# Optimization experiments

Measured on AMD Instinct MI355X. Metric: run time of the kernel, lower is better.

Reference implementation:

```python
import jax, jax.numpy as jnp
import numpy as np

B, T, D, H, E, L = 128, 200, 256, 4, 4, 2
HD = D // H
ITEM = 50000


def _ln(x, s, b):
    m = x.mean(-1, keepdims=True)
    v = ((x - m) ** 2).mean(-1, keepdims=True)
    return (x - m) / jnp.sqrt(v + 1e-8) * s + b


def setup_inputs() -> dict:
    key = jax.random.key(0)
    ks = jax.random.split(key, 20)
    n = lambda k, sh: jax.random.normal(k, sh, jnp.float32) * 0.02
    inp = {}
    inp['log_seqs'] = jax.random.randint(ks[0], (B, T), 0, ITEM + 1)
    inp['pos_seqs'] = jax.random.randint(ks[1], (B, T), 0, ITEM + 1)
    inp['neg_seqs'] = jax.random.randint(ks[2], (B, T), 0, ITEM + 1)
    inp['expert_ids'] = jax.random.randint(ks[3], (B,), 0, E)
    inp['item_emb'] = n(ks[4], (ITEM + 1, D)).at[0].set(0.0)  # padding_idx=0
    inp['pos_emb'] = n(ks[5], (T + 1, D)).at[0].set(0.0)
    inp['attn_ln_s'] = jnp.ones((L, D), jnp.float32)
    inp['attn_ln_b'] = jnp.zeros((L, D), jnp.float32)
    inp['in_w'] = n(ks[6], (L, E, 3 * D, D))
    inp['in_b'] = jnp.zeros((L, E, 3 * D), jnp.float32)
    inp['out_w'] = n(ks[7], (L, E, D, D))
    inp['out_b'] = jnp.zeros((L, E, D), jnp.float32)
    inp['fwd_ln_s'] = jnp.ones((L, D), jnp.float32)
    inp['fwd_ln_b'] = jnp.zeros((L, D), jnp.float32)
    inp['ffn_w1'] = n(ks[8], (L, D, D))
    inp['ffn_b1'] = jnp.zeros((L, D), jnp.float32)
    inp['ffn_w2'] = n(ks[9], (L, D, D))
    inp['ffn_b2'] = jnp.zeros((L, D), jnp.float32)
    inp['last_ln_s'] = jnp.ones((D,), jnp.float32)
    inp['last_ln_b'] = jnp.zeros((D,), jnp.float32)
    return inp


def reference(log_seqs, pos_seqs, neg_seqs, expert_ids, item_emb, pos_emb,
              attn_ln_s, attn_ln_b, in_w, in_b, out_w, out_b,
              fwd_ln_s, fwd_ln_b, ffn_w1, ffn_b1, ffn_w2, ffn_b2,
              last_ln_s, last_ln_b):
    seqs = item_emb[log_seqs] * jnp.float32(np.sqrt(D))          # [B,T,D]
    poss = jnp.arange(1, T + 1)[None, :] * (log_seqs != 0)       # pos ids, 0 where pad
    seqs = seqs + pos_emb[poss]
    causal = jnp.tril(jnp.ones((T, T), bool))
    scale = jnp.float32(1.0 / np.sqrt(HD))

    for l in range(L):
        qn = _ln(seqs, attn_ln_s[l], attn_ln_b[l])               # query is LN'd; K,V are not
        wq, wk, wv = in_w[l, :, :D], in_w[l, :, D:2 * D], in_w[l, :, 2 * D:]
        bq, bk, bv = in_b[l, :, :D], in_b[l, :, D:2 * D], in_b[l, :, 2 * D:]
        q = jnp.einsum('btd,efd->ebtf', qn, wq) + bq[:, None, None, :]
        k = jnp.einsum('btd,efd->ebtf', seqs, wk) + bk[:, None, None, :]
        v = jnp.einsum('btd,efd->ebtf', seqs, wv) + bv[:, None, None, :]
        q = q.reshape(E, B, T, H, HD)
        k = k.reshape(E, B, T, H, HD)
        v = v.reshape(E, B, T, H, HD)
        scores = jnp.einsum('ebqhd,ebkhd->ebhqk', q, k) * scale  # [E,B,H,T,T]
        scores = jnp.where(causal, scores, jnp.float32(-1e9))
        attn = jax.nn.softmax(scores, axis=-1)
        o = jnp.einsum('ebhqk,ebkhd->ebqhd', attn, v).reshape(E, B, T, D)
        o = jnp.einsum('ebtd,efd->ebtf', o, out_w[l]) + out_b[l][:, None, None, :]
        gated = o[expert_ids, jnp.arange(B)]                     # hard one-hot gate -> [B,T,D]
        seqs = qn + gated
        seqs = _ln(seqs, fwd_ln_s[l], fwd_ln_b[l])
        h = jax.nn.relu(seqs @ ffn_w1[l].T + ffn_b1[l])
        seqs = seqs + (h @ ffn_w2[l].T + ffn_b2[l])

    feats = _ln(seqs, last_ln_s, last_ln_b)                      # [B,T,D]
    pos_logits = (feats * item_emb[pos_seqs]).sum(-1)            # [B,T]
    neg_logits = (feats * item_emb[neg_seqs]).sum(-1)
    return (pos_logits, neg_logits)
```

## Files before the change

kernel.cpp:

```cpp
#include <hip/hip_runtime.h>
#include <hip/hip_bf16.h>

namespace {

typedef unsigned short ushort;
constexpr int B  = 128;
constexpr int T  = 200;
constexpr int D  = 256;
constexpr int H  = 4;
constexpr int NE = 4;
constexpr int NL = 2;
constexpr int HD = 64;
constexpr int BT = B * T;

constexpr int BM = 64;
constexpr int BK = 64;
constexpr int MT = (T + BM - 1) / BM;
constexpr int HS = 264;

typedef __bf16 bf16x8 __attribute__((ext_vector_type(8)));
typedef float f32x4 __attribute__((ext_vector_type(4)));
typedef unsigned short ushort8v __attribute__((ext_vector_type(8)));

__device__ inline float wave_sum(float x) {
#pragma unroll
  for (int off = 32; off > 0; off >>= 1) x += __shfl_xor(x, off);
  return x;
}
__device__ inline unsigned int f2bf(float x) {
  unsigned int u = __float_as_uint(x);
  return (u + 0x7fffu + ((u >> 16) & 1u)) >> 16;
}
__device__ inline ushort f2bfs(float x) { return (ushort)f2bf(x); }
__device__ inline float bf2f(ushort u) {
  return __uint_as_float((unsigned int)u << 16);
}
__device__ inline bf16x8 ldb8(const ushort* p) {
  return __builtin_bit_cast(bf16x8, *(const ushort8v*)p);
}

__global__ void k_cvt(const float* __restrict__ src, ushort* __restrict__ dst,
                      int n4) {
  int i = blockIdx.x * 256 + threadIdx.x;
  if (i < n4) {
    float4 v = ((const float4*)src)[i];
    ushort4 u;
    u.x = f2bfs(v.x); u.y = f2bfs(v.y); u.z = f2bfs(v.z); u.w = f2bfs(v.w);
    ((ushort4*)dst)[i] = u;
  }
}

__global__ __launch_bounds__(256) void k_embed_ln(
    const int* __restrict__ log_seqs, const float* __restrict__ item_emb,
    const float* __restrict__ pos_emb, const float* __restrict__ lns,
    const float* __restrict__ lnb, ushort* __restrict__ seqs,
    ushort* __restrict__ qn) {
  int tok = blockIdx.x * 4 + (threadIdx.x >> 6);
  int lane = threadIdx.x & 63;
  int t = tok % T;
  int idx = log_seqs[tok];
  int pos = (idx != 0) ? (t + 1) : 0;
  float4 iv = ((const float4*)(item_emb + (size_t)idx * D))[lane];
  float4 pv = ((const float4*)(pos_emb + (size_t)pos * D))[lane];
  float v0 = iv.x * 16.0f + pv.x;
  float v1 = iv.y * 16.0f + pv.y;
  float v2 = iv.z * 16.0f + pv.z;
  float v3 = iv.w * 16.0f + pv.w;
  ushort4 r;
  r.x = f2bfs(v0); r.y = f2bfs(v1); r.z = f2bfs(v2); r.w = f2bfs(v3);
  ((ushort4*)(seqs + (size_t)tok * D))[lane] = r;
  float mean = wave_sum(v0 + v1 + v2 + v3) * (1.0f / D);
  float c0 = v0 - mean, c1 = v1 - mean, c2 = v2 - mean, c3 = v3 - mean;
  float var = wave_sum(c0 * c0 + c1 * c1 + c2 * c2 + c3 * c3) * (1.0f / D);
  float inv = rsqrtf(var + 1e-8f);
  float4 sv = ((const float4*)lns)[lane];
  float4 bv = ((const float4*)lnb)[lane];
  ushort4 o;
  o.x = f2bfs(c0 * inv * sv.x + bv.x);
  o.y = f2bfs(c1 * inv * sv.y + bv.y);
  o.z = f2bfs(c2 * inv * sv.z + bv.z);
  o.w = f2bfs(c3 * inv * sv.w + bv.w);
  ((ushort4*)(qn + (size_t)tok * D))[lane] = o;
}

template <int ROWS>
__device__ inline void stage_bf16(const ushort* __restrict__ src, int ld,
                                  int valid, int k0, ushort* __restrict__ dst,
                                  int tid) {
#pragma unroll
  for (int p = 0; p < ROWS * 8 / 256; p++) {
    int slot = p * 256 + tid;
    int r = slot >> 3, s_st = slot & 7;
    int s_src = s_st ^ (r & 7);
    int rs = (r < valid) ? r : (valid - 1);
    uint4 w = *(const uint4*)(src + (size_t)rs * ld + k0 + s_src * 8);
    *(uint4*)(dst + r * BK + s_st * 8) = w;
  }
}
__device__ inline bf16x8 frag(const ushort* tile, int row, int slot_log) {
  int s = slot_log ^ (row & 7);
  return ldb8(tile + row * BK + s * 8);
}

__global__ __launch_bounds__(256) void k_gemm_qkv(
    const ushort* __restrict__ qn, const ushort* __restrict__ seqs,
    const ushort* __restrict__ w, const float* __restrict__ bias,
    const int* __restrict__ expert_ids,
    ushort* __restrict__ q, ushort* __restrict__ k, ushort* __restrict__ v) {
  constexpr int NWG = B * MT * 6;
  int phys = blockIdx.x;
  int bid = (phys & 7) * (NWG >> 3) + (phys >> 3);
  int nt = bid % 6;
  int mt = (bid / 6) % MT;
  int b  = bid / (6 * MT);
  int e = expert_ids[b];
  int m0 = mt * BM;
  int valid = min(BM, T - m0);
  const ushort* X = (nt < 2) ? qn : seqs;
  const ushort* Xb = X + (size_t)(b * T + m0) * D;
  const ushort* Wb = w + (size_t)e * 3 * D * D + (size_t)nt * 128 * D;

  __shared__ __align__(16) ushort Xl[BM * BK];
  __shared__ __align__(16) ushort Wl[128 * BK];
  int tid = threadIdx.x, wv = tid >> 6, lane = tid & 63;
  int g = lane >> 4, lm = lane & 15;

  f32x4 acc[4][2];
#pragma unroll
  for (int mi = 0; mi < 4; mi++)
#pragma unroll
    for (int ni = 0; ni < 2; ni++) acc[mi][ni] = (f32x4){0.f, 0.f, 0.f, 0.f};

  for (int kt = 0; kt < D / BK; kt++) {
    stage_bf16<BM>(Xb, D, valid, kt * BK, Xl, tid);
    stage_bf16<128>(Wb, D, 128, kt * BK, Wl, tid);
    __syncthreads();
    bf16x8 a[4][2], bb[2][2];
#pragma unroll
    for (int mi = 0; mi < 4; mi++)
#pragma unroll
      for (int hh = 0; hh < 2; hh++)
        a[mi][hh] = frag(Xl, mi * 16 + lm, hh * 4 + g);
#pragma unroll
    for (int ni = 0; ni < 2; ni++)
#pragma unroll
      for (int hh = 0; hh < 2; hh++)
        bb[ni][hh] = frag(Wl, wv * 32 + ni * 16 + lm, hh * 4 + g);
#pragma unroll
    for (int mi = 0; mi < 4; mi++)
#pragma unroll
      for (int ni = 0; ni < 2; ni++) {
        acc[mi][ni] = __builtin_amdgcn_mfma_f32_16x16x32_bf16(a[mi][0], bb[ni][0],
                                                              acc[mi][ni], 0, 0, 0);
        acc[mi][ni] = __builtin_amdgcn_mfma_f32_16x16x32_bf16(a[mi][1], bb[ni][1],
                                                              acc[mi][ni], 0, 0, 0);
      }
    __syncthreads();
  }

  ushort* outb = (nt < 2) ? q : (nt < 4 ? k : v);
  size_t rowbase = (size_t)(b * T + m0);
#pragma unroll
  for (int mi = 0; mi < 4; mi++) {
#pragma unroll
    for (int ni = 0; ni < 2; ni++) {
      int col = (nt & 1) * 128 + wv * 32 + ni * 16 + lm;
      float bbv = bias[e * 3 * D + nt * 128 + wv * 32 + ni * 16 + lm];
#pragma unroll
      for (int r = 0; r < 4; r++) {
        int lr = mi * 16 + 4 * g + r;
        if (lr < valid)
          outb[(rowbase + lr) * D + col] = f2bfs(acc[mi][ni][r] + bbv);
      }
    }
  }
}

__global__ __launch_bounds__(256) void k_oproj(
    const ushort* __restrict__ o, const ushort* __restrict__ qn,
    const ushort* __restrict__ w, const float* __restrict__ bo,
    const float* __restrict__ lns, const float* __restrict__ lnb,
    const int* __restrict__ expert_ids, ushort* __restrict__ seqs) {
  int bid = blockIdx.x;
  int mt = bid % MT;
  int b  = bid / MT;
  int e = expert_ids[b];
  int m0 = mt * BM;
  int valid = min(BM, T - m0);
  const ushort* Xb = o + (size_t)(b * T + m0) * D;
  const ushort* Wb = w + (size_t)e * D * D;

  __shared__ __align__(16) ushort Xl[BM * BK];
  __shared__ __align__(16) ushort Wl[D * BK];
  __shared__ float rs_sum[BM][4];
  __shared__ float rs_sq[BM][4];
  int tid = threadIdx.x, wv = tid >> 6, lane = tid & 63;
  int g = lane >> 4, lm = lane & 15;

  f32x4 acc[4][4];
#pragma unroll
  for (int mi = 0; mi < 4; mi++)
#pragma unroll
    for (int ni = 0; ni < 4; ni++) acc[mi][ni] = (f32x4){0.f, 0.f, 0.f, 0.f};

  for (int kt = 0; kt < D / BK; kt++) {
    stage_bf16<BM>(Xb, D, valid, kt * BK, Xl, tid);
    stage_bf16<D>(Wb, D, D, kt * BK, Wl, tid);
    __syncthreads();
    bf16x8 a[4][2], bb[4][2];
#pragma unroll
    for (int mi = 0; mi < 4; mi++)
#pragma unroll
      for (int hh = 0; hh < 2; hh++)
        a[mi][hh] = frag(Xl, mi * 16 + lm, hh * 4 + g);
#pragma unroll
    for (int ni = 0; ni < 4; ni++)
#pragma unroll
      for (int hh = 0; hh < 2; hh++)
        bb[ni][hh] = frag(Wl, wv * 64 + ni * 16 + lm, hh * 4 + g);
#pragma unroll
    for (int mi = 0; mi < 4; mi++)
#pragma unroll
      for (int ni = 0; ni < 4; ni++) {
        acc[mi][ni] = __builtin_amdgcn_mfma_f32_16x16x32_bf16(a[mi][0], bb[ni][0],
                                                              acc[mi][ni], 0, 0, 0);
        acc[mi][ni] = __builtin_amdgcn_mfma_f32_16x16x32_bf16(a[mi][1], bb[ni][1],
                                                              acc[mi][ni], 0, 0, 0);
      }
    __syncthreads();
  }

  size_t rowbase = (size_t)(b * T + m0);
#pragma unroll
  for (int ni = 0; ni < 4; ni++) {
    int col = wv * 64 + ni * 16 + lm;
    float bbv = bo[e * D + col];
#pragma unroll
    for (int mi = 0; mi < 4; mi++)
#pragma unroll
      for (int r = 0; r < 4; r++) {
        int lr = mi * 16 + 4 * g + r;
        int lrc = (lr < valid) ? lr : (valid - 1);
        acc[mi][ni][r] += bbv + bf2f(qn[(rowbase + lrc) * D + col]);
      }
  }
#pragma unroll
  for (int mi = 0; mi < 4; mi++)
#pragma unroll
    for (int r = 0; r < 4; r++) {
      float s = 0.f, q2 = 0.f;
#pragma unroll
      for (int ni = 0; ni < 4; ni++) {
        float x = acc[mi][ni][r];
        s += x; q2 += x * x;
      }
#pragma unroll
      for (int off = 1; off < 16; off <<= 1) {
        s += __shfl_xor(s, off);
        q2 += __shfl_xor(q2, off);
      }
      if (lm == 0) {
        int row = mi * 16 + 4 * g + r;
        rs_sum[row][wv] = s;
        rs_sq[row][wv] = q2;
      }
    }
  __syncthreads();
  float scv[4], bcv[4];
#pragma unroll
  for (int ni = 0; ni < 4; ni++) {
    int col = wv * 64 + ni * 16 + lm;
    scv[ni] = lns[col];
    bcv[ni] = lnb[col];
  }
#pragma unroll
  for (int mi = 0; mi < 4; mi++)
#pragma unroll
    for (int r = 0; r < 4; r++) {
      int lr = mi * 16 + 4 * g + r;
      float4 s4 = *(const float4*)rs_sum[lr];
      float4 q4 = *(const float4*)rs_sq[lr];
      float mean = (s4.x + s4.y + s4.z + s4.w) * (1.0f / D);
      float var = (q4.x + q4.y + q4.z + q4.w) * (1.0f / D) - mean * mean;
      float rstd = rsqrtf(fmaxf(var, 0.f) + 1e-8f);
      if (lr < valid) {
#pragma unroll
        for (int ni = 0; ni < 4; ni++) {
          int col = wv * 64 + ni * 16 + lm;
          float lnv = (acc[mi][ni][r] - mean) * rstd * scv[ni] + bcv[ni];
          seqs[(rowbase + lr) * D + col] = f2bfs(lnv);
        }
      }
    }
}

__global__ __launch_bounds__(256) void k_ffn(
    const ushort* __restrict__ xin, const ushort* __restrict__ w1,
    const float* __restrict__ b1, const ushort* __restrict__ w2,
    const float* __restrict__ b2, const float* __restrict__ lns,
    const float* __restrict__ lnb, ushort* __restrict__ seqs,
    ushort* __restrict__ qn) {
  int bid = blockIdx.x;
  int mt = bid % MT;
  int b  = bid / MT;
  int m0 = mt * BM;
  int valid = min(BM, T - m0);
  const ushort* Xb = xin + (size_t)(b * T + m0) * D;

  __shared__ __align__(16) ushort Xl[BM * BK];
  __shared__ __align__(16) ushort Wl[D * BK];
  __shared__ __align__(16) ushort hl[BM * HS];
  __shared__ float rs_sum[BM][4];
  __shared__ float rs_sq[BM][4];
  int tid = threadIdx.x, wv = tid >> 6, lane = tid & 63;
  int g = lane >> 4, lm = lane & 15;
  size_t rowbase = (size_t)(b * T + m0);

  f32x4 acc[4][4];
#pragma unroll
  for (int mi = 0; mi < 4; mi++)
#pragma unroll
    for (int ni = 0; ni < 4; ni++) acc[mi][ni] = (f32x4){0.f, 0.f, 0.f, 0.f};

  for (int kt = 0; kt < D / BK; kt++) {
    stage_bf16<BM>(Xb, D, valid, kt * BK, Xl, tid);
    stage_bf16<D>(w1, D, D, kt * BK, Wl, tid);
    __syncthreads();
    bf16x8 a[4][2], bb[4][2];
#pragma unroll
    for (int mi = 0; mi < 4; mi++)
#pragma unroll
      for (int hh = 0; hh < 2; hh++)
        a[mi][hh] = frag(Xl, mi * 16 + lm, hh * 4 + g);
#pragma unroll
    for (int ni = 0; ni < 4; ni++)
#pragma unroll
      for (int hh = 0; hh < 2; hh++)
        bb[ni][hh] = frag(Wl, wv * 64 + ni * 16 + lm, hh * 4 + g);
#pragma unroll
    for (int mi = 0; mi < 4; mi++)
#pragma unroll
      for (int ni = 0; ni < 4; ni++) {
        acc[mi][ni] = __builtin_amdgcn_mfma_f32_16x16x32_bf16(a[mi][0], bb[ni][0],
                                                              acc[mi][ni], 0, 0, 0);
        acc[mi][ni] = __builtin_amdgcn_mfma_f32_16x16x32_bf16(a[mi][1], bb[ni][1],
                                                              acc[mi][ni], 0, 0, 0);
      }
    __syncthreads();
  }
#pragma unroll
  for (int ni = 0; ni < 4; ni++) {
    int col = wv * 64 + ni * 16 + lm;
    float bbv = b1[col];
#pragma unroll
    for (int mi = 0; mi < 4; mi++)
#pragma unroll
      for (int r = 0; r < 4; r++) {
        int row = mi * 16 + 4 * g + r;
        hl[row * HS + col] = f2bfs(fmaxf(acc[mi][ni][r] + bbv, 0.f));
      }
  }
#pragma unroll
  for (int mi = 0; mi < 4; mi++)
#pragma unroll
    for (int ni = 0; ni < 4; ni++) acc[mi][ni] = (f32x4){0.f, 0.f, 0.f, 0.f};
  for (int kt = 0; kt < D / BK; kt++) {
    stage_bf16<D>(w2, D, D, kt * BK, Wl, tid);
    __syncthreads();
    bf16x8 a[4][2], bb[4][2];
#pragma unroll
    for (int mi = 0; mi < 4; mi++)
#pragma unroll
      for (int hh = 0; hh < 2; hh++)
        a[mi][hh] = ldb8(&hl[(mi * 16 + lm) * HS + kt * BK + hh * 32 + 8 * g]);
#pragma unroll
    for (int ni = 0; ni < 4; ni++)
#pragma unroll
      for (int hh = 0; hh < 2; hh++)
        bb[ni][hh] = frag(Wl, wv * 64 + ni * 16 + lm, hh * 4 + g);
#pragma unroll
    for (int mi = 0; mi < 4; mi++)
#pragma unroll
      for (int ni = 0; ni < 4; ni++) {
        acc[mi][ni] = __builtin_amdgcn_mfma_f32_16x16x32_bf16(a[mi][0], bb[ni][0],
                                                              acc[mi][ni], 0, 0, 0);
        acc[mi][ni] = __builtin_amdgcn_mfma_f32_16x16x32_bf16(a[mi][1], bb[ni][1],
                                                              acc[mi][ni], 0, 0, 0);
      }
    __syncthreads();
  }
#pragma unroll
  for (int ni = 0; ni < 4; ni++) {
    int col = wv * 64 + ni * 16 + lm;
    float bbv = b2[col];
#pragma unroll
    for (int mi = 0; mi < 4; mi++)
#pragma unroll
      for (int r = 0; r < 4; r++) {
        int lr = mi * 16 + 4 * g + r;
        int lrc = (lr < valid) ? lr : (valid - 1);
        acc[mi][ni][r] += bbv + bf2f(xin[(rowbase + lrc) * D + col]);
      }
  }
#pragma unroll
  for (int mi = 0; mi < 4; mi++)
#pragma unroll
    for (int r = 0; r < 4; r++) {
      float s = 0.f, q2 = 0.f;
#pragma unroll
      for (int ni = 0; ni < 4; ni++) {
        float x = acc[mi][ni][r];
        s += x; q2 += x * x;
      }
#pragma unroll
      for (int off = 1; off < 16; off <<= 1) {
        s += __shfl_xor(s, off);
        q2 += __shfl_xor(q2, off);
      }
      if (lm == 0) {
        int row = mi * 16 + 4 * g + r;
        rs_sum[row][wv] = s;
        rs_sq[row][wv] = q2;
      }
    }
  __syncthreads();
  float scv[4], bcv[4];
#pragma unroll
  for (int ni = 0; ni < 4; ni++) {
    int col = wv * 64 + ni * 16 + lm;
    scv[ni] = lns[col];
    bcv[ni] = lnb[col];
  }
#pragma unroll
  for (int mi = 0; mi < 4; mi++)
#pragma unroll
    for (int r = 0; r < 4; r++) {
      int lr = mi * 16 + 4 * g + r;
      float4 s4 = *(const float4*)rs_sum[lr];
      float4 q4 = *(const float4*)rs_sq[lr];
      float mean = (s4.x + s4.y + s4.z + s4.w) * (1.0f / D);
      float var = (q4.x + q4.y + q4.z + q4.w) * (1.0f / D) - mean * mean;
      float rstd = rsqrtf(fmaxf(var, 0.f) + 1e-8f);
      if (lr < valid) {
#pragma unroll
        for (int ni = 0; ni < 4; ni++) {
          int col = wv * 64 + ni * 16 + lm;
          float val = acc[mi][ni][r];
          size_t idx = (rowbase + lr) * D + col;
          seqs[idx] = f2bfs(val);
          qn[idx] = f2bfs((val - mean) * rstd * scv[ni] + bcv[ni]);
        }
      }
    }
}

constexpr int KROWS = 224;
constexpr int KSS = 72;
constexpr int VSS = 232;
constexpr int PSS = 40;
__global__ __launch_bounds__(256) void k_attn(const ushort* __restrict__ q,
                                              const ushort* __restrict__ k,
                                              const ushort* __restrict__ v,
                                              ushort* __restrict__ o) {
  int bh = blockIdx.x;
  int b = bh >> 2, h = bh & 3;
  __shared__ __align__(16) ushort Kl[KROWS][KSS];
  __shared__ __align__(16) ushort Vt[HD][VSS];
  __shared__ __align__(16) ushort Pl[4][16][PSS];
  const size_t base = (size_t)b * T * D + h * HD;
  int tid = threadIdx.x, wave = tid >> 6, lane = tid & 63;
  int g = lane >> 4, lm = lane & 15;

#pragma unroll
  for (int p = 0; p < 7; p++) {
    int slot = p * 256 + tid;
    int key = slot >> 3, s8 = (slot & 7) << 3;
    uint4 w = make_uint4(0, 0, 0, 0);
    if (key < T) w = *(const uint4*)(k + base + (size_t)key * D + s8);
    *(uint4*)&Kl[key][s8] = w;
  }
#pragma unroll
  for (int p = 0; p < 28; p++) {
    int slot = p * 256 + tid;
    int key = slot >> 5, dp = (slot & 31) << 1;
    unsigned int w = 0;
    if (key < T) w = *(const unsigned int*)(v + base + (size_t)key * D + dp);
    Vt[dp][key] = (ushort)(w & 0xffffu);
    Vt[dp + 1][key] = (ushort)(w >> 16);
  }
  __syncthreads();

  const unsigned long long SCHED = 0x0189D27AD36BD45CULL;
  unsigned sch = (unsigned)(SCHED >> (wave * 16)) & 0xFFFFu;
  const float sc = 0.125f * 1.44269504f;

  for (int si = 0; si < 4; si++) {
    int qt = (sch >> (si * 4)) & 15;
    if (qt > 12) break;
    int row = qt * 16 + lm;
    int qrow = min(row, T - 1);
    const ushort* qr = q + base + (size_t)qrow * D;
    bf16x8 qf0 = ldb8(qr + 8 * g);
    bf16x8 qf1 = ldb8(qr + 32 + 8 * g);

    f32x4 oacc[4];
#pragma unroll
    for (int dt = 0; dt < 4; dt++) oacc[dt] = (f32x4){0.f, 0.f, 0.f, 0.f};
    float mrun = -3e38f, lsum = 0.f;

    int nch = qt / 2 + 1;
    for (int c = 0; c < nch; c++) {
      int kb = c * 32;
      f32x4 s01[2];
#pragma unroll
      for (int t = 0; t < 2; t++) {
        int krow = kb + t * 16 + lm;
        bf16x8 a0 = ldb8(&Kl[krow][8 * g]);
        bf16x8 a1 = ldb8(&Kl[krow][32 + 8 * g]);
        f32x4 z = (f32x4){0.f, 0.f, 0.f, 0.f};
        z = __builtin_amdgcn_mfma_f32_16x16x32_bf16(a0, qf0, z, 0, 0, 0);
        z = __builtin_amdgcn_mfma_f32_16x16x32_bf16(a1, qf1, z, 0, 0, 0);
        s01[t] = z;
      }
      float sv[8];
      float mx = -3e38f;
#pragma unroll
      for (int t = 0; t < 2; t++)
#pragma unroll
        for (int r = 0; r < 4; r++) {
          int key = kb + t * 16 + 4 * g + r;
          float x = (key <= row) ? s01[t][r] * sc : -3e38f;
          sv[t * 4 + r] = x;
          mx = fmaxf(mx, x);
        }
      mx = fmaxf(mx, __shfl_xor(mx, 16));
      mx = fmaxf(mx, __shfl_xor(mx, 32));
      float mnew = fmaxf(mrun, mx);
      float corr = __builtin_amdgcn_exp2f(mrun - mnew);
      float ps = 0.f;
      ushort8v pu;
#pragma unroll
      for (int i = 0; i < 8; i++) {
        float p = __builtin_amdgcn_exp2f(sv[i] - mnew);
        ps += p;
        pu[i] = f2bfs(p);
      }
      ps += __shfl_xor(ps, 16);
      ps += __shfl_xor(ps, 32);
      lsum = lsum * corr + ps;
      mrun = mnew;
      *(ushort4*)&Pl[wave][lm][4 * g]      = ((ushort4*)&pu)[0];
      *(ushort4*)&Pl[wave][lm][16 + 4 * g] = ((ushort4*)&pu)[1];
#pragma unroll
      for (int dt = 0; dt < 4; dt++)
#pragma unroll
        for (int r = 0; r < 4; r++) oacc[dt][r] *= corr;
      bf16x8 pf = ldb8(&Pl[wave][lm][8 * g]);
#pragma unroll
      for (int dt = 0; dt < 4; dt++) {
        bf16x8 av = ldb8(&Vt[dt * 16 + lm][kb + 8 * g]);
        oacc[dt] = __builtin_amdgcn_mfma_f32_16x16x32_bf16(av, pf, oacc[dt], 0, 0, 0);
      }
    }

    if (row < T) {
      float rinv = 1.0f / lsum;
      ushort* orow = o + base + (size_t)row * D;
#pragma unroll
      for (int dt = 0; dt < 4; dt++) {
        ushort4 uo;
        uo.x = f2bfs(oacc[dt][0] * rinv);
        uo.y = f2bfs(oacc[dt][1] * rinv);
        uo.z = f2bfs(oacc[dt][2] * rinv);
        uo.w = f2bfs(oacc[dt][3] * rinv);
        *(ushort4*)(orow + dt * 16 + 4 * g) = uo;
      }
    }
  }
}

__global__ __launch_bounds__(256) void k_final(const ushort* __restrict__ seqs,
                                               const float* __restrict__ sc,
                                               const float* __restrict__ bi,
                                               const int* __restrict__ pos_seqs,
                                               const int* __restrict__ neg_seqs,
                                               const float* __restrict__ item_emb,
                                               float* __restrict__ out) {
  int tok = blockIdx.x * 4 + (threadIdx.x >> 6);
  int lane = threadIdx.x & 63;
  ushort4 xu = ((const ushort4*)(seqs + (size_t)tok * D))[lane];
  float x0 = bf2f(xu.x), x1 = bf2f(xu.y), x2 = bf2f(xu.z), x3 = bf2f(xu.w);
  float mean = wave_sum(x0 + x1 + x2 + x3) * (1.0f / D);
  float c0 = x0 - mean, c1 = x1 - mean, c2 = x2 - mean, c3 = x3 - mean;
  float var = wave_sum(c0 * c0 + c1 * c1 + c2 * c2 + c3 * c3) * (1.0f / D);
  float inv = rsqrtf(var + 1e-8f);
  float4 sv = ((const float4*)sc)[lane];
  float4 bv = ((const float4*)bi)[lane];
  float f0 = c0 * inv * sv.x + bv.x;
  float f1 = c1 * inv * sv.y + bv.y;
  float f2 = c2 * inv * sv.z + bv.z;
  float f3 = c3 * inv * sv.w + bv.w;
  int ip = pos_seqs[tok];
  int in_ = neg_seqs[tok];
  float4 pe = ((const float4*)(item_emb + (size_t)ip * D))[lane];
  float4 ne = ((const float4*)(item_emb + (size_t)in_ * D))[lane];
  float dp = wave_sum(f0 * pe.x + f1 * pe.y + f2 * pe.z + f3 * pe.w);
  float dn = wave_sum(f0 * ne.x + f1 * ne.y + f2 * ne.z + f3 * ne.w);
  if (lane == 0) {
    out[tok] = dp;
    out[BT + tok] = dn;
  }
}

}

extern "C" void kernel_launch(void* const* d_in, const int* in_sizes, int n_in,
                              void* d_out, int out_size, void* d_ws, size_t ws_size,
                              hipStream_t stream) {
  const int*   log_seqs   = (const int*)d_in[0];
  const int*   pos_seqs   = (const int*)d_in[1];
  const int*   neg_seqs   = (const int*)d_in[2];
  const int*   expert_ids = (const int*)d_in[3];
  const float* item_emb   = (const float*)d_in[4];
  const float* pos_emb    = (const float*)d_in[5];
  const float* attn_ln_s  = (const float*)d_in[6];
  const float* attn_ln_b  = (const float*)d_in[7];
  const float* in_w       = (const float*)d_in[8];
  const float* in_b       = (const float*)d_in[9];
  const float* out_w      = (const float*)d_in[10];
  const float* out_b      = (const float*)d_in[11];
  const float* fwd_ln_s   = (const float*)d_in[12];
  const float* fwd_ln_b   = (const float*)d_in[13];
  const float* ffn_w1     = (const float*)d_in[14];
  const float* ffn_b1     = (const float*)d_in[15];
  const float* ffn_w2     = (const float*)d_in[16];
  const float* ffn_b2     = (const float*)d_in[17];
  const float* last_ln_s  = (const float*)d_in[18];
  const float* last_ln_b  = (const float*)d_in[19];
  float* out = (float*)d_out;

  const size_t N = (size_t)BT * D;
  ushort* seqs = (ushort*)d_ws;
  ushort* qn   = seqs + N;
  ushort* q    = qn + N;
  ushort* kbuf = q + N;
  ushort* vbuf = kbuf + N;
  ushort* obuf = kbuf;
  ushort* wqkv = vbuf + N;
  ushort* wout = wqkv + (size_t)NL * NE * 3 * D * D;
  ushort* wf1  = wout + (size_t)NL * NE * D * D;
  ushort* wf2  = wf1 + (size_t)NL * D * D;

  {
    int n4a = NL * NE * 3 * D * D / 4;
    int n4b = NL * NE * D * D / 4;
    int n4c = NL * D * D / 4;
    k_cvt<<<(n4a + 255) / 256, 256, 0, stream>>>(in_w, wqkv, n4a);
    k_cvt<<<(n4b + 255) / 256, 256, 0, stream>>>(out_w, wout, n4b);
    k_cvt<<<(n4c + 255) / 256, 256, 0, stream>>>(ffn_w1, wf1, n4c);
    k_cvt<<<(n4c + 255) / 256, 256, 0, stream>>>(ffn_w2, wf2, n4c);
  }

  k_embed_ln<<<BT / 4, 256, 0, stream>>>(log_seqs, item_emb, pos_emb,
                                         attn_ln_s, attn_ln_b, seqs, qn);

  for (int l = 0; l < NL; l++) {
    int ln_next = (l + 1 < NL) ? (l + 1) : l;
    k_gemm_qkv<<<B * MT * 6, 256, 0, stream>>>(
        qn, seqs, wqkv + (size_t)l * NE * 3 * D * D,
        in_b + (size_t)l * NE * 3 * D, expert_ids, q, kbuf, vbuf);
    k_attn<<<B * H, 256, 0, stream>>>(q, kbuf, vbuf, obuf);
    k_oproj<<<B * MT, 256, 0, stream>>>(
        obuf, qn, wout + (size_t)l * NE * D * D, out_b + (size_t)l * NE * D,
        fwd_ln_s + (size_t)l * D, fwd_ln_b + (size_t)l * D, expert_ids, seqs);
    k_ffn<<<B * MT, 256, 0, stream>>>(
        seqs, wf1 + (size_t)l * D * D, ffn_b1 + (size_t)l * D,
        wf2 + (size_t)l * D * D, ffn_b2 + (size_t)l * D,
        attn_ln_s + (size_t)ln_next * D, attn_ln_b + (size_t)ln_next * D,
        seqs, qn);
  }

  k_final<<<BT / 4, 256, 0, stream>>>(seqs, last_ln_s, last_ln_b, pos_seqs,
                                      neg_seqs, item_emb, out);
}
```

Measured before the change: 261.7 us.

## Fuse out-projection, LayerNorm and FFN into one 512-thread kernel; merge weight conversions

Merges the out-projection with residual and LayerNorm and the two-layer FFN into a single kernel. The normalized activations and the FFN hidden layer stay in swizzled shared memory, so the global round-trip of seqs between the two kernels goes away. Blocks grow to 512 threads arranged as a 2x4 wave grid, and the four weight-conversion launches become one. The cost is about 80KB of LDS per block and launch bounds of 512,2, which may limit occupancy.

```diff
diff --git a/kernel.cpp b/kernel.cpp
--- a/kernel.cpp
+++ b/kernel.cpp
@@ -16,7 +16,6 @@
 constexpr int BM = 64;
 constexpr int BK = 64;
 constexpr int MT = (T + BM - 1) / BM;
-constexpr int HS = 264;
 
 typedef __bf16 bf16x8 __attribute__((ext_vector_type(8)));
 typedef float f32x4 __attribute__((ext_vector_type(4)));
@@ -39,15 +38,21 @@
   return __builtin_bit_cast(bf16x8, *(const ushort8v*)p);
 }
 
-__global__ void k_cvt(const float* __restrict__ src, ushort* __restrict__ dst,
-                      int n4) {
+__global__ void k_cvt_all(const float* __restrict__ a, const float* __restrict__ b,
+                          const float* __restrict__ c, const float* __restrict__ d,
+                          ushort* __restrict__ dst, int nA4, int nB4, int nC4) {
   int i = blockIdx.x * 256 + threadIdx.x;
-  if (i < n4) {
-    float4 v = ((const float4*)src)[i];
-    ushort4 u;
-    u.x = f2bfs(v.x); u.y = f2bfs(v.y); u.z = f2bfs(v.z); u.w = f2bfs(v.w);
-    ((ushort4*)dst)[i] = u;
-  }
+  int nAB = nA4 + nB4, nABC = nAB + nC4, tot = nABC + nC4;
+  if (i >= tot) return;
+  const float* src; int j;
+  if (i < nA4)       { src = a; j = i; }
+  else if (i < nAB)  { src = b; j = i - nA4; }
+  else if (i < nABC) { src = c; j = i - nAB; }
+  else               { src = d; j = i - nABC; }
+  float4 v = ((const float4*)src)[j];
+  ushort4 u;
+  u.x = f2bfs(v.x); u.y = f2bfs(v.y); u.z = f2bfs(v.z); u.w = f2bfs(v.w);
+  ((ushort4*)dst)[i] = u;
 }
 
 __global__ __launch_bounds__(256) void k_embed_ln(
@@ -97,9 +102,31 @@
     *(uint4*)(dst + r * BK + s_st * 8) = w;
   }
 }
+template <int ROWS>
+__device__ inline void stage512(const ushort* __restrict__ src, int ld,
+                                int valid, int k0, ushort* __restrict__ dst,
+                                int tid) {
+#pragma unroll
+  for (int p = 0; p < ROWS * 8 / 512; p++) {
+    int slot = p * 512 + tid;
+    int r = slot >> 3, s_st = slot & 7;
+    int s_src = s_st ^ (r & 7);
+    int rs = (r < valid) ? r : (valid - 1);
+    uint4 w = *(const uint4*)(src + (size_t)rs * ld + k0 + s_src * 8);
+    *(uint4*)(dst + r * BK + s_st * 8) = w;
+  }
+}
 __device__ inline bf16x8 frag(const ushort* tile, int row, int slot_log) {
   int s = slot_log ^ (row & 7);
   return ldb8(tile + row * BK + s * 8);
+}
+__device__ inline bf16x8 frag256(const ushort* tile, int row, int k0, int slot_log) {
+  int s = slot_log ^ (row & 7);
+  return ldb8(tile + row * 256 + k0 + s * 8);
+}
+__device__ inline int swz256(int row, int col) {
+  int s = ((col >> 3) & 7) ^ (row & 7);
+  return row * 256 + (col & ~63) + s * 8 + (col & 7);
 }
 
 __global__ __launch_bounds__(256) void k_gemm_qkv(
@@ -176,50 +203,58 @@
   }
 }
 
-__global__ __launch_bounds__(256) void k_oproj(
+__global__ __launch_bounds__(512, 2) void k_postattn(
     const ushort* __restrict__ o, const ushort* __restrict__ qn,
-    const ushort* __restrict__ w, const float* __restrict__ bo,
-    const float* __restrict__ lns, const float* __restrict__ lnb,
-    const int* __restrict__ expert_ids, ushort* __restrict__ seqs) {
+    const ushort* __restrict__ wo, const float* __restrict__ bo,
+    const float* __restrict__ lns1, const float* __restrict__ lnb1,
+    const ushort* __restrict__ w1, const float* __restrict__ b1,
+    const ushort* __restrict__ w2, const float* __restrict__ b2,
+    const float* __restrict__ lns2, const float* __restrict__ lnb2,
+    const int* __restrict__ expert_ids,
+    ushort* __restrict__ seqs, ushort* __restrict__ qno) {
   int bid = blockIdx.x;
   int mt = bid % MT;
   int b  = bid / MT;
   int e = expert_ids[b];
   int m0 = mt * BM;
   int valid = min(BM, T - m0);
-  const ushort* Xb = o + (size_t)(b * T + m0) * D;
-  const ushort* Wb = w + (size_t)e * D * D;
-
-  __shared__ __align__(16) ushort Xl[BM * BK];
+  size_t rowbase = (size_t)(b * T + m0);
+  const ushort* Ob = o + rowbase * D;
+  const ushort* We = wo + (size_t)e * D * D;
+
+  __shared__ __align__(16) ushort XnL[BM * 256];
   __shared__ __align__(16) ushort Wl[D * BK];
+  __shared__ __align__(16) ushort U[BM * 256];
   __shared__ float rs_sum[BM][4];
   __shared__ float rs_sq[BM][4];
+
   int tid = threadIdx.x, wv = tid >> 6, lane = tid & 63;
+  int wr = wv >> 2, wc = wv & 3;
   int g = lane >> 4, lm = lane & 15;
 
-  f32x4 acc[4][4];
-#pragma unroll
-  for (int mi = 0; mi < 4; mi++)
+  f32x4 acc[2][4];
+#pragma unroll
+  for (int mi = 0; mi < 2; mi++)
 #pragma unroll
     for (int ni = 0; ni < 4; ni++) acc[mi][ni] = (f32x4){0.f, 0.f, 0.f, 0.f};
 
   for (int kt = 0; kt < D / BK; kt++) {
-    stage_bf16<BM>(Xb, D, valid, kt * BK, Xl, tid);
-    stage_bf16<D>(Wb, D, D, kt * BK, Wl, tid);
-    __syncthreads();
-    bf16x8 a[4][2], bb[4][2];
-#pragma unroll
-    for (int mi = 0; mi < 4; mi++)
-#pragma unroll
-      for (int hh = 0; hh < 2; hh++)
-        a[mi][hh] = frag(Xl, mi * 16 + lm, hh * 4 + g);
+    stage512<BM>(Ob, D, valid, kt * BK, U, tid);
+    stage512<D>(We, D, D, kt * BK, Wl, tid);
+    __syncthreads();
+    bf16x8 a[2][2], bb[4][2];
+#pragma unroll
+    for (int mi = 0; mi < 2; mi++)
+#pragma unroll
+      for (int hh = 0; hh < 2; hh++)
+        a[mi][hh] = frag(U, wr * 32 + mi * 16 + lm, hh * 4 + g);
 #pragma unroll
     for (int ni = 0; ni < 4; ni++)
 #pragma unroll
       for (int hh = 0; hh < 2; hh++)
-        bb[ni][hh] = frag(Wl, wv * 64 + ni * 16 + lm, hh * 4 + g);
-#pragma unroll
-    for (int mi = 0; mi < 4; mi++)
+        bb[ni][hh] = frag(Wl, wc * 64 + ni * 16 + lm, hh * 4 + g);
+#pragma unroll
+    for (int mi = 0; mi < 2; mi++)
 #pragma unroll
       for (int ni = 0; ni < 4; ni++) {
         acc[mi][ni] = __builtin_amdgcn_mfma_f32_16x16x32_bf16(a[mi][0], bb[ni][0],
@@ -229,23 +264,21 @@
       }
     __syncthreads();
   }
-
-  size_t rowbase = (size_t)(b * T + m0);
 #pragma unroll
   for (int ni = 0; ni < 4; ni++) {
-    int col = wv * 64 + ni * 16 + lm;
+    int col = wc * 64 + ni * 16 + lm;
     float bbv = bo[e * D + col];
 #pragma unroll
-    for (int mi = 0; mi < 4; mi++)
+    for (int mi = 0; mi < 2; mi++)
 #pragma unroll
       for (int r = 0; r < 4; r++) {
-        int lr = mi * 16 + 4 * g + r;
+        int lr = wr * 32 + mi * 16 + 4 * g + r;
         int lrc = (lr < valid) ? lr : (valid - 1);
         acc[mi][ni][r] += bbv + bf2f(qn[(rowbase + lrc) * D + col]);
       }
   }
 #pragma unroll
-  for (int mi = 0; mi < 4; mi++)
+  for (int mi = 0; mi < 2; mi++)
 #pragma unroll
     for (int r = 0; r < 4; r++) {
       float s = 0.f, q2 = 0.f;
@@ -260,85 +293,60 @@
         q2 += __shfl_xor(q2, off);
       }
       if (lm == 0) {
-        int row = mi * 16 + 4 * g + r;
-        rs_sum[row][wv] = s;
-        rs_sq[row][wv] = q2;
+        int row = wr * 32 + mi * 16 + 4 * g + r;
+        rs_sum[row][wc] = s;
+        rs_sq[row][wc] = q2;
       }
     }
   __syncthreads();
-  float scv[4], bcv[4];
-#pragma unroll
-  for (int ni = 0; ni < 4; ni++) {
-    int col = wv * 64 + ni * 16 + lm;
-    scv[ni] = lns[col];
-    bcv[ni] = lnb[col];
-  }
-#pragma unroll
-  for (int mi = 0; mi < 4; mi++)
-#pragma unroll
-    for (int r = 0; r < 4; r++) {
-      int lr = mi * 16 + 4 * g + r;
-      float4 s4 = *(const float4*)rs_sum[lr];
-      float4 q4 = *(const float4*)rs_sq[lr];
-      float mean = (s4.x + s4.y + s4.z + s4.w) * (1.0f / D);
-      float var = (q4.x + q4.y + q4.z + q4.w) * (1.0f / D) - mean * mean;
-      float rstd = rsqrtf(fmaxf(var, 0.f) + 1e-8f);
-      if (lr < valid) {
+  {
+    float scv[4], bcv[4];
+#pragma unroll
+    for (int ni = 0; ni < 4; ni++) {
+      int col = wc * 64 + ni * 16 + lm;
+      scv[ni] = lns1[col];
+      bcv[ni] = lnb1[col];
+    }
+#pragma unroll
+    for (int mi = 0; mi < 2; mi++)
+#pragma unroll
+      for (int r = 0; r < 4; r++) {
+        int lr = wr * 32 + mi * 16 + 4 * g + r;
+        float4 s4 = *(const float4*)rs_sum[lr];
+        float4 q4 = *(const float4*)rs_sq[lr];
+        float mean = (s4.x + s4.y + s4.z + s4.w) * (1.0f / D);
+        float var = (q4.x + q4.y + q4.z + q4.w) * (1.0f / D) - mean * mean;
+        float rstd = rsqrtf(fmaxf(var, 0.f) + 1e-8f);
 #pragma unroll
         for (int ni = 0; ni < 4; ni++) {
-          int col = wv * 64 + ni * 16 + lm;
-          float lnv = (acc[mi][ni][r] - mean) * rstd * scv[ni] + bcv[ni];
-          seqs[(rowbase + lr) * D + col] = f2bfs(lnv);
+          int col = wc * 64 + ni * 16 + lm;
+          float xn = (acc[mi][ni][r] - mean) * rstd * scv[ni] + bcv[ni];
+          XnL[swz256(lr, col)] = f2bfs(xn);
         }
       }
-    }
-}
-
-__global__ __launch_bounds__(256) void k_ffn(
-    const ushort* __restrict__ xin, const ushort* __restrict__ w1,
-    const float* __restrict__ b1, const ushort* __restrict__ w2,
-    const float* __restrict__ b2, const float* __restrict__ lns,
-    const float* __restrict__ lnb, ushort* __restrict__ seqs,
-    ushort* __restrict__ qn) {
-  int bid = blockIdx.x;
-  int mt = bid % MT;
-  int b  = bid / MT;
-  int m0 = mt * BM;
-  int valid = min(BM, T - m0);
-  const ushort* Xb = xin + (size_t)(b * T + m0) * D;
-
-  __shared__ __align__(16) ushort Xl[BM * BK];
-  __shared__ __align__(16) ushort Wl[D * BK];
-  __shared__ __align__(16) ushort hl[BM * HS];
-  __shared__ float rs_sum[BM][4];
-  __shared__ float rs_sq[BM][4];
-  int tid = threadIdx.x, wv = tid >> 6, lane = tid & 63;
-  int g = lane >> 4, lm = lane & 15;
-  size_t rowbase = (size_t)(b * T + m0);
-
-  f32x4 acc[4][4];
-#pragma unroll
-  for (int mi = 0; mi < 4; mi++)
+  }
+  __syncthreads();
+
+#pragma unroll
+  for (int mi = 0; mi < 2; mi++)
 #pragma unroll
     for (int ni = 0; ni < 4; ni++) acc[mi][ni] = (f32x4){0.f, 0.f, 0.f, 0.f};
-
   for (int kt = 0; kt < D / BK; kt++) {
-    stage_bf16<BM>(Xb, D, valid, kt * BK, Xl, tid);
-    stage_bf16<D>(w1, D, D, kt * BK, Wl, tid);
-    __syncthreads();
-    bf16x8 a[4][2], bb[4][2];
-#pragma unroll
-    for (int mi = 0; mi < 4; mi++)
-#pragma unroll
-      for (int hh = 0; hh < 2; hh++)
-        a[mi][hh] = frag(Xl, mi * 16 + lm, hh * 4 + g);
+    stage512<D>(w1, D, D, kt * BK, Wl, tid);
+    __syncthreads();
+    bf16x8 a[2][2], bb[4][2];
+#pragma unroll
+    for (int mi = 0; mi < 2; mi++)
+#pragma unroll
+      for (int hh = 0; hh < 2; hh++)
+        a[mi][hh] = frag256(XnL, wr * 32 + mi * 16 + lm, kt * BK, hh * 4 + g);
 #pragma unroll
     for (int ni = 0; ni < 4; ni++)
 #pragma unroll
       for (int hh = 0; hh < 2; hh++)
-        bb[ni][hh] = frag(Wl, wv * 64 + ni * 16 + lm, hh * 4 + g);
-#pragma unroll
-    for (int mi = 0; mi < 4; mi++)
+        bb[ni][hh] = frag(Wl, wc * 64 + ni * 16 + lm, hh * 4 + g);
+#pragma unroll
+    for (int mi = 0; mi < 2; mi++)
 #pragma unroll
       for (int ni = 0; ni < 4; ni++) {
         acc[mi][ni] = __builtin_amdgcn_mfma_f32_16x16x32_bf16(a[mi][0], bb[ni][0],
@@ -350,36 +358,38 @@
   }
 #pragma unroll
   for (int ni = 0; ni < 4; ni++) {
-    int col = wv * 64 + ni * 16 + lm;
+    int col = wc * 64 + ni * 16 + lm;
     float bbv = b1[col];
 #pragma unroll
-    for (int mi = 0; mi < 4; mi++)
+    for (int mi = 0; mi < 2; mi++)
 #pragma unroll
       for (int r = 0; r < 4; r++) {
-        int row = mi * 16 + 4 * g + r;
-        hl[row * HS + col] = f2bfs(fmaxf(acc[mi][ni][r] + bbv, 0.f));
-      }
-  }
-#pragma unroll
-  for (int mi = 0; mi < 4; mi++)
+        int row = wr * 32 + mi * 16 + 4 * g + r;
+        U[swz256(row, col)] = f2bfs(fmaxf(acc[mi][ni][r] + bbv, 0.f));
+      }
+  }
+  __syncthreads();
+
+#pragma unroll
+  for (int mi = 0; mi < 2; mi++)
 #pragma unroll
     for (int ni = 0; ni < 4; ni++) acc[mi][ni] = (f32x4){0.f, 0.f, 0.f, 0.f};
   for (int kt = 0; kt < D / BK; kt++) {
-    stage_bf16<D>(w2, D, D, kt * BK, Wl, tid);
-    __syncthreads();
-    bf16x8 a[4][2], bb[4][2];
-#pragma unroll
-    for (int mi = 0; mi < 4; mi++)
-#pragma unroll
-      for (int hh = 0; hh < 2; hh++)
-        a[mi][hh] = ldb8(&hl[(mi * 16 + lm) * HS + kt * BK + hh * 32 + 8 * g]);
+    stage512<D>(w2, D, D, kt * BK, Wl, tid);
+    __syncthreads();
+    bf16x8 a[2][2], bb[4][2];
+#pragma unroll
+    for (int mi = 0; mi < 2; mi++)
+#pragma unroll
+      for (int hh = 0; hh < 2; hh++)
+        a[mi][hh] = frag256(U, wr * 32 + mi * 16 + lm, kt * BK, hh * 4 + g);
 #pragma unroll
     for (int ni = 0; ni < 4; ni++)
 #pragma unroll
       for (int hh = 0; hh < 2; hh++)
-        bb[ni][hh] = frag(Wl, wv * 64 + ni * 16 + lm, hh * 4 + g);
-#pragma unroll
-    for (int mi = 0; mi < 4; mi++)
+        bb[ni][hh] = frag(Wl, wc * 64 + ni * 16 + lm, hh * 4 + g);
+#pragma unroll
+    for (int mi = 0; mi < 2; mi++)
 #pragma unroll
       for (int ni = 0; ni < 4; ni++) {
         acc[mi][ni] = __builtin_amdgcn_mfma_f32_16x16x32_bf16(a[mi][0], bb[ni][0],
@@ -391,19 +401,18 @@
   }
 #pragma unroll
   for (int ni = 0; ni < 4; ni++) {
-    int col = wv * 64 + ni * 16 + lm;
+    int col = wc * 64 + ni * 16 + lm;
     float bbv = b2[col];
 #pragma unroll
-    for (int mi = 0; mi < 4; mi++)
+    for (int mi = 0; mi < 2; mi++)
 #pragma unroll
       for (int r = 0; r < 4; r++) {
-        int lr = mi * 16 + 4 * g + r;
-        int lrc = (lr < valid) ? lr : (valid - 1);
-        acc[mi][ni][r] += bbv + bf2f(xin[(rowbase + lrc) * D + col]);
-      }
-  }
-#pragma unroll
-  for (int mi = 0; mi < 4; mi++)
+        int row = wr * 32 + mi * 16 + 4 * g + r;
+        acc[mi][ni][r] += bbv + bf2f(XnL[swz256(row, col)]);
+      }
+  }
+#pragma unroll
+  for (int mi = 0; mi < 2; mi++)
 #pragma unroll
     for (int r = 0; r < 4; r++) {
       float s = 0.f, q2 = 0.f;
@@ -418,40 +427,42 @@
         q2 += __shfl_xor(q2, off);
       }
       if (lm == 0) {
-        int row = mi * 16 + 4 * g + r;
-        rs_sum[row][wv] = s;
-        rs_sq[row][wv] = q2;
+        int row = wr * 32 + mi * 16 + 4 * g + r;
+        rs_sum[row][wc] = s;
+        rs_sq[row][wc] = q2;
       }
     }
   __syncthreads();
-  float scv[4], bcv[4];
-#pragma unroll
-  for (int ni = 0; ni < 4; ni++) {
-    int col = wv * 64 + ni * 16 + lm;
-    scv[ni] = lns[col];
-    bcv[ni] = lnb[col];
-  }
-#pragma unroll
-  for (int mi = 0; mi < 4; mi++)
-#pragma unroll
-    for (int r = 0; r < 4; r++) {
-      int lr = mi * 16 + 4 * g + r;
-      float4 s4 = *(const float4*)rs_sum[lr];
-      float4 q4 = *(const float4*)rs_sq[lr];
-      float mean = (s4.x + s4.y + s4.z + s4.w) * (1.0f / D);
-      float var = (q4.x + q4.y + q4.z + q4.w) * (1.0f / D) - mean * mean;
-      float rstd = rsqrtf(fmaxf(var, 0.f) + 1e-8f);
-      if (lr < valid) {
-#pragma unroll
-        for (int ni = 0; ni < 4; ni++) {
-          int col = wv * 64 + ni * 16 + lm;
-          float val = acc[mi][ni][r];
-          size_t idx = (rowbase + lr) * D + col;
-          seqs[idx] = f2bfs(val);
-          qn[idx] = f2bfs((val - mean) * rstd * scv[ni] + bcv[ni]);
+  {
+    float scv[4], bcv[4];
+#pragma unroll
+    for (int ni = 0; ni < 4; ni++) {
+      int col = wc * 64 + ni * 16 + lm;
+      scv[ni] = lns2[col];
+      bcv[ni] = lnb2[col];
+    }
+#pragma unroll
+    for (int mi = 0; mi < 2; mi++)
+#pragma unroll
+      for (int r = 0; r < 4; r++) {
+        int lr = wr * 32 + mi * 16 + 4 * g + r;
+        float4 s4 = *(const float4*)rs_sum[lr];
+        float4 q4 = *(const float4*)rs_sq[lr];
+        float mean = (s4.x + s4.y + s4.z + s4.w) * (1.0f / D);
+        float var = (q4.x + q4.y + q4.z + q4.w) * (1.0f / D) - mean * mean;
+        float rstd = rsqrtf(fmaxf(var, 0.f) + 1e-8f);
+        if (lr < valid) {
+#pragma unroll
+          for (int ni = 0; ni < 4; ni++) {
+            int col = wc * 64 + ni * 16 + lm;
+            float val = acc[mi][ni][r];
+            size_t idx = (rowbase + lr) * D + col;
+            seqs[idx] = f2bfs(val);
+            qno[idx] = f2bfs((val - mean) * rstd * scv[ni] + bcv[ni]);
+          }
         }
       }
-    }
+  }
 }
 
 constexpr int KROWS = 224;
@@ -652,13 +663,12 @@
   ushort* wf2  = wf1 + (size_t)NL * D * D;
 
   {
-    int n4a = NL * NE * 3 * D * D / 4;
-    int n4b = NL * NE * D * D / 4;
-    int n4c = NL * D * D / 4;
-    k_cvt<<<(n4a + 255) / 256, 256, 0, stream>>>(in_w, wqkv, n4a);
-    k_cvt<<<(n4b + 255) / 256, 256, 0, stream>>>(out_w, wout, n4b);
-    k_cvt<<<(n4c + 255) / 256, 256, 0, stream>>>(ffn_w1, wf1, n4c);
-    k_cvt<<<(n4c + 255) / 256, 256, 0, stream>>>(ffn_w2, wf2, n4c);
+    int nA4 = NL * NE * 3 * D * D / 4;
+    int nB4 = NL * NE * D * D / 4;
+    int nC4 = NL * D * D / 4;
+    int tot = nA4 + nB4 + 2 * nC4;
+    k_cvt_all<<<(tot + 255) / 256, 256, 0, stream>>>(in_w, out_w, ffn_w1, ffn_w2,
+                                                     wqkv, nA4, nB4, nC4);
   }
 
   k_embed_ln<<<BT / 4, 256, 0, stream>>>(log_seqs, item_emb, pos_emb,
@@ -670,14 +680,13 @@
         qn, seqs, wqkv + (size_t)l * NE * 3 * D * D,
         in_b + (size_t)l * NE * 3 * D, expert_ids, q, kbuf, vbuf);
     k_attn<<<B * H, 256, 0, stream>>>(q, kbuf, vbuf, obuf);
-    k_oproj<<<B * MT, 256, 0, stream>>>(
+    k_postattn<<<B * MT, 512, 0, stream>>>(
         obuf, qn, wout + (size_t)l * NE * D * D, out_b + (size_t)l * NE * D,
-        fwd_ln_s + (size_t)l * D, fwd_ln_b + (size_t)l * D, expert_ids, seqs);
-    k_ffn<<<B * MT, 256, 0, stream>>>(
-        seqs, wf1 + (size_t)l * D * D, ffn_b1 + (size_t)l * D,
+        fwd_ln_s + (size_t)l * D, fwd_ln_b + (size_t)l * D,
+        wf1 + (size_t)l * D * D, ffn_b1 + (size_t)l * D,
         wf2 + (size_t)l * D * D, ffn_b2 + (size_t)l * D,
         attn_ln_s + (size_t)ln_next * D, attn_ln_b + (size_t)ln_next * D,
-        seqs, qn);
+        expert_ids, seqs, qn);
   }
 
   k_final<<<BT / 4, 256, 0, stream>>>(seqs, last_ln_s, last_ln_b, pos_seqs,
```

After: 221.3 us. -15.4%, faster.
